# Kernel optimization log

Measured on AMD Instinct MI355X. Metric: run time of the kernel, lower is better.

The kernel has to match this reference:

```python
import jax, jax.numpy as jnp
import numpy as np

B, F, M, C = 4096, 2048, 14, 100
K = 2 ** M  # 16384 latent binary codes


def _codebook(m):
    # itertools.product([0,1], repeat=m) order: row i is binary repr of i, MSB first
    i = jnp.arange(2 ** m)
    j = jnp.arange(m)
    return ((i[:, None] >> (m - 1 - j)[None, :]) & 1).astype(jnp.float32)  # [K, m]


def setup_inputs() -> dict:
    key = jax.random.key(0)
    k1, k2, k3, k4, k5, k6 = jax.random.split(key, 6)
    init_a = 2.0 / np.sqrt(F)
    init_b = 2.0 / np.sqrt(M)
    return {
        "x_in": jax.random.normal(k1, (B, F), dtype=jnp.float32),
        "y_in": jax.random.randint(k2, (B,), 0, C),
        "alpha_0": jax.random.normal(k3, (M,), dtype=jnp.float32),
        "alpha": init_a * jax.random.normal(k4, (M, F), dtype=jnp.float32),
        "beta_0": jax.random.normal(k5, (C,), dtype=jnp.float32),
        "beta": init_b * jax.random.normal(k6, (C, M), dtype=jnp.float32),
    }


def reference(x_in, y_in, alpha_0, alpha, beta_0, beta):
    cb = _codebook(M)  # [K, M]
    # linear_eta
    le = alpha_0[None, :] + x_in @ alpha.T  # [B, M]
    # linear_pi over all codes (mod_codes = 2*cb - 1)
    linear_pi = beta_0[:, None] + beta @ (2.0 * cb - 1.0).T  # [C, K]
    pi = jax.nn.softmax(linear_pi, axis=0)  # exp / sum over classes
    # P(Z|X): exp(cb @ le.T - sum_j softplus(le)) transposed -> [B, K]
    sp = jax.nn.softplus(le)  # log(1 + exp(le)), stable  [B, M]
    P_ZgivenX = jnp.exp((cb @ le.T - jnp.sum(sp, axis=1)[None, :]).T)  # [B, K]
    y1 = jax.nn.one_hot(y_in, C, dtype=le.dtype)  # [B, C]
    numerator = (y1 @ pi) * P_ZgivenX  # [B, K]
    denom = jnp.sum(numerator, axis=1)  # [B]
    # E[Ind Z_j]: masked sum over codes with bit j == 1 == single matmul with cb
    E_IndZ = (numerator @ cb) / denom[:, None]  # [B, M]
    # EI
    EZ = 2.0 * E_IndZ - 1.0
    EI = jnp.sum(y1 * (beta_0[None, :] + EZ @ beta.T))
    # EII
    prob_log = numerator / denom[:, None]
    log_terms = jax.scipy.special.logsumexp(linear_pi, axis=0)  # [K]
    EII = jnp.sum(prob_log * log_terms[None, :])
    # EIII, EIV
    EIII = jnp.sum(E_IndZ * le)
    EIV = jnp.sum(sp)
    return EI - EII + EIII - EIV
```

## Files before the change

kernel.cpp:

```cpp
#include <hip/hip_runtime.h>
#include <math.h>

#define NB 4096
#define NF 2048
#define NM 14
#define NC 100
#define NK 16384

__device__ __forceinline__ float softplus_f(float v) {
    return fmaxf(v, 0.f) + log1pf(__expf(-fabsf(v)));
}

extern "C" __global__ void __launch_bounds__(256) k1_le(
        const float* __restrict__ x, const float* __restrict__ alpha,
        float* __restrict__ le_part) {
    const int tid = threadIdx.x;
    const int wave = tid >> 6, lane = tid & 63;
    const int grp = blockIdx.x >> 1;
    const int half = blockIdx.x & 1;
    const int row0 = grp * 16 + wave * 4;
    const float4* __restrict__ x4 = (const float4*)x;
    const float4* __restrict__ a4 = (const float4*)alpha;
    float acc[4][NM];
#pragma unroll
    for (int r = 0; r < 4; ++r)
#pragma unroll
        for (int j = 0; j < NM; ++j) acc[r][j] = 0.f;
#pragma unroll 1
    for (int cc = 0; cc < 4; ++cc) {
        const int f4i = half * 256 + cc * 64 + lane;
        float4 av[NM];
#pragma unroll
        for (int j = 0; j < NM; ++j) av[j] = a4[j * 512 + f4i];
#pragma unroll
        for (int r = 0; r < 4; ++r) {
            const float4 xv = x4[(row0 + r) * 512 + f4i];
#pragma unroll
            for (int j = 0; j < NM; ++j) {
                acc[r][j] = fmaf(xv.x, av[j].x, acc[r][j]);
                acc[r][j] = fmaf(xv.y, av[j].y, acc[r][j]);
                acc[r][j] = fmaf(xv.z, av[j].z, acc[r][j]);
                acc[r][j] = fmaf(xv.w, av[j].w, acc[r][j]);
            }
        }
    }
#pragma unroll
    for (int m = 1; m < 64; m <<= 1) {
#pragma unroll
        for (int r = 0; r < 4; ++r)
#pragma unroll
            for (int j = 0; j < NM; ++j)
                acc[r][j] += __shfl_xor(acc[r][j], m, 64);
    }
    if (lane == 0) {
        float* dst = le_part + half * (NB * NM) + row0 * NM;
#pragma unroll
        for (int r = 0; r < 4; ++r)
#pragma unroll
            for (int j = 0; j < NM; ++j)
                dst[r * NM + j] = acc[r][j];
    }
}

extern "C" __global__ void __launch_bounds__(256) k2_sl(
        const float* __restrict__ beta, const float* __restrict__ beta0,
        float2* __restrict__ SL) {
    __shared__ float b2[NC * NM];
    __shared__ float base_s[NC];
    __shared__ float Sp[4][64];
    const int tid = threadIdx.x;
    for (int i = tid; i < NC * NM; i += 256) b2[i] = 2.f * beta[i];
    if (tid < NC) {
        float s = beta0[tid];
        for (int j = 0; j < NM; ++j) s -= beta[tid * NM + j];
        base_s[tid] = s;
    }
    __syncthreads();
    const int kl = tid & 63, q = tid >> 6;
    const int k = blockIdx.x * 64 + kl;
    float bits[NM];
#pragma unroll
    for (int j = 0; j < NM; ++j) bits[j] = (float)((k >> (13 - j)) & 1);
    float S = 0.f;
    for (int c = q * 25; c < q * 25 + 25; ++c) {
        float d = base_s[c];
#pragma unroll
        for (int j = 0; j < NM; ++j) d = fmaf(bits[j], b2[c * NM + j], d);
        S += __expf(d);
    }
    Sp[q][kl] = S;
    __syncthreads();
    if (tid < 64) {
        const float Sf = Sp[0][tid] + Sp[1][tid] + Sp[2][tid] + Sp[3][tid];
        SL[blockIdx.x * 64 + tid] = make_float2(1.f / Sf, __logf(Sf));
    }
}

extern "C" __global__ void __launch_bounds__(256) k3_main(
        const float* __restrict__ le_part, const float* __restrict__ alpha0,
        const int* __restrict__ y, const float* __restrict__ beta,
        const float* __restrict__ beta0, const float2* __restrict__ SL,
        float* __restrict__ partial) {
    __shared__ float t_s[8][16];
    __shared__ float sp_s[8][16];
    __shared__ float cs_s[8];
    __shared__ float f_s[8];
    __shared__ float Alds[128][8];
    __shared__ float Elds[128][8];
    __shared__ float red[4][16];
    const int tid = threadIdx.x;
    const int b0 = blockIdx.x * 8;

    if (tid < 128) {
        const int r = tid >> 4, j = tid & 15;
        if (j < NM) {
            const int yv = y[b0 + r];
            const float lv = le_part[(b0 + r) * NM + j]
                           + le_part[NB * NM + (b0 + r) * NM + j] + alpha0[j];
            t_s[r][j] = lv + 2.f * beta[yv * NM + j];
            sp_s[r][j] = softplus_f(lv);
        }
    }
    __syncthreads();
    if (tid < 8) {
        const int yv = y[b0 + tid];
        float cs = beta0[yv];
        for (int j = 0; j < NM; ++j) {
            cs -= beta[yv * NM + j];
            cs += fmaxf(t_s[tid][j], 0.f) - sp_s[tid][j];
        }
        cs_s[tid] = cs;
    }
#pragma unroll
    for (int e = 0; e < 4; ++e) {
        const int idx = tid + 256 * e;
        const int r = idx & 7, h = idx >> 3;
        float A = 0.f, ub = 0.f;
#pragma unroll
        for (int j = 0; j < 7; ++j) {
            const float tv = t_s[r][j];
            A += ((h >> (6 - j)) & 1) ? tv : 0.f;
            ub += fmaxf(tv, 0.f);
        }
        const float Ap = A - ub;
        Alds[h][r] = Ap;
        Elds[h][r] = __expf(Ap);
    }
    const int l = tid & 127;
    float eb[8], aterm[8];
#pragma unroll
    for (int r = 0; r < 8; ++r) {
        float A = 0.f, ub = 0.f;
#pragma unroll
        for (int j = 7; j < NM; ++j) {
            const float tv = t_s[r][j];
            A += ((l >> (13 - j)) & 1) ? tv : 0.f;
            ub += fmaxf(tv, 0.f);
        }
        aterm[r] = A - ub;
        eb[r] = __expf(A - ub);
    }
    __syncthreads();

    float U[8], V[8];
#pragma unroll
    for (int r = 0; r < 8; ++r) { U[r] = 0.f; V[r] = 0.f; }
    const int c = tid >> 7;
#pragma unroll 4
    for (int i = 0; i < 64; ++i) {
        const float2 sl = SL[i * 256 + tid];
        const int h = 2 * i + c;
        const float4 Aa = *(const float4*)&Alds[h][0];
        const float4 Ab = *(const float4*)&Alds[h][4];
        const float4 Ea = *(const float4*)&Elds[h][0];
        const float4 Eb = *(const float4*)&Elds[h][4];
        const float Ar[8] = {Aa.x, Aa.y, Aa.z, Aa.w, Ab.x, Ab.y, Ab.z, Ab.w};
        const float Er[8] = {Ea.x, Ea.y, Ea.z, Ea.w, Eb.x, Eb.y, Eb.z, Eb.w};
#pragma unroll
        for (int r = 0; r < 8; ++r) {
            const float rest = Er[r] * sl.x;
            U[r] += rest;
            V[r] = fmaf(rest, Ar[r] - sl.y, V[r]);
        }
    }
    float vals[16];
#pragma unroll
    for (int r = 0; r < 8; ++r) {
        vals[r] = eb[r] * U[r];
        vals[8 + r] = eb[r] * fmaf(aterm[r], U[r], V[r]);
    }
#pragma unroll
    for (int m = 1; m < 64; m <<= 1)
#pragma unroll
        for (int q2 = 0; q2 < 16; ++q2)
            vals[q2] += __shfl_xor(vals[q2], m, 64);
    const int wv = tid >> 6, lane = tid & 63;
    if (lane == 0) {
#pragma unroll
        for (int q2 = 0; q2 < 16; ++q2) red[wv][q2] = vals[q2];
    }
    __syncthreads();
    if (tid < 16)
        red[0][tid] = red[0][tid] + red[1][tid] + red[2][tid] + red[3][tid];
    __syncthreads();
    if (tid < 8)
        f_s[tid] = cs_s[tid] + red[0][8 + tid] / red[0][tid];
    __syncthreads();
    if (tid == 0) {
        float s = 0.f;
#pragma unroll
        for (int r = 0; r < 8; ++r) s += f_s[r];
        partial[blockIdx.x] = s;
    }
}

extern "C" __global__ void __launch_bounds__(256) k4_reduce(
        const float* __restrict__ partial, float* __restrict__ out) {
    __shared__ float red[4];
    const int tid = threadIdx.x;
    float s = partial[tid] + partial[tid + 256];
#pragma unroll
    for (int m = 1; m < 64; m <<= 1) s += __shfl_xor(s, m, 64);
    const int wv = tid >> 6, lane = tid & 63;
    if (lane == 0) red[wv] = s;
    __syncthreads();
    if (tid == 0) out[0] = red[0] + red[1] + red[2] + red[3];
}

extern "C" void kernel_launch(void* const* d_in, const int* in_sizes, int n_in,
                              void* d_out, int out_size, void* d_ws, size_t ws_size,
                              hipStream_t stream) {
    const float* x      = (const float*)d_in[0];
    const int*   y      = (const int*)d_in[1];
    const float* alpha0 = (const float*)d_in[2];
    const float* alpha  = (const float*)d_in[3];
    const float* beta0  = (const float*)d_in[4];
    const float* beta   = (const float*)d_in[5];

    char* ws = (char*)d_ws;
    float*  le_part = (float*)ws;
    float2* SL      = (float2*)(ws + 2 * NB * NM * 4);
    float*  partial = (float*)(ws + 2 * NB * NM * 4 + NK * 8);
    float*  out     = (float*)d_out;

    k1_le<<<512, 256, 0, stream>>>(x, alpha, le_part);
    k2_sl<<<256, 256, 0, stream>>>(beta, beta0, SL);
    k3_main<<<512, 256, 0, stream>>>(le_part, alpha0, y, beta, beta0, SL, partial);
    k4_reduce<<<1, 256, 0, stream>>>(partial, out);
}
```

Before: 122.8 us.

## Merge le and SL kernels, fold final reduce into main, drop Alds

Merges the linear_eta GEMV and the per-code log-sum-exp kernels into one launch split by block index, and replaces the separate reduce kernel with a last-block atomic-counter reduction inside the main kernel. In the main loop it stops loading the A values from shared memory. It instead accumulates per-bit masked sums of the probabilities and rebuilds the V term algebraically after the loop. This removes two launches and halves the LDS traffic in the hot loop, at the cost of more registers (M[6][8]) and a full unroll that may lower occupancy.

```diff
diff --git a/kernel.cpp b/kernel.cpp
--- a/kernel.cpp
+++ b/kernel.cpp
@@ -11,88 +11,90 @@
     return fmaxf(v, 0.f) + log1pf(__expf(-fabsf(v)));
 }
 
-extern "C" __global__ void __launch_bounds__(256) k1_le(
+extern "C" __global__ void __launch_bounds__(256) k12(
         const float* __restrict__ x, const float* __restrict__ alpha,
-        float* __restrict__ le_part) {
-    const int tid = threadIdx.x;
-    const int wave = tid >> 6, lane = tid & 63;
-    const int grp = blockIdx.x >> 1;
-    const int half = blockIdx.x & 1;
-    const int row0 = grp * 16 + wave * 4;
-    const float4* __restrict__ x4 = (const float4*)x;
-    const float4* __restrict__ a4 = (const float4*)alpha;
-    float acc[4][NM];
-#pragma unroll
-    for (int r = 0; r < 4; ++r)
-#pragma unroll
-        for (int j = 0; j < NM; ++j) acc[r][j] = 0.f;
-#pragma unroll 1
-    for (int cc = 0; cc < 4; ++cc) {
-        const int f4i = half * 256 + cc * 64 + lane;
-        float4 av[NM];
-#pragma unroll
-        for (int j = 0; j < NM; ++j) av[j] = a4[j * 512 + f4i];
-#pragma unroll
-        for (int r = 0; r < 4; ++r) {
-            const float4 xv = x4[(row0 + r) * 512 + f4i];
-#pragma unroll
-            for (int j = 0; j < NM; ++j) {
-                acc[r][j] = fmaf(xv.x, av[j].x, acc[r][j]);
-                acc[r][j] = fmaf(xv.y, av[j].y, acc[r][j]);
-                acc[r][j] = fmaf(xv.z, av[j].z, acc[r][j]);
-                acc[r][j] = fmaf(xv.w, av[j].w, acc[r][j]);
-            }
-        }
-    }
-#pragma unroll
-    for (int m = 1; m < 64; m <<= 1) {
-#pragma unroll
-        for (int r = 0; r < 4; ++r)
-#pragma unroll
-            for (int j = 0; j < NM; ++j)
-                acc[r][j] += __shfl_xor(acc[r][j], m, 64);
-    }
-    if (lane == 0) {
-        float* dst = le_part + half * (NB * NM) + row0 * NM;
-#pragma unroll
-        for (int r = 0; r < 4; ++r)
-#pragma unroll
-            for (int j = 0; j < NM; ++j)
-                dst[r * NM + j] = acc[r][j];
-    }
-}
-
-extern "C" __global__ void __launch_bounds__(256) k2_sl(
         const float* __restrict__ beta, const float* __restrict__ beta0,
-        float2* __restrict__ SL) {
+        float* __restrict__ le_part, float2* __restrict__ SL,
+        int* __restrict__ counter) {
     __shared__ float b2[NC * NM];
     __shared__ float base_s[NC];
     __shared__ float Sp[4][64];
     const int tid = threadIdx.x;
-    for (int i = tid; i < NC * NM; i += 256) b2[i] = 2.f * beta[i];
-    if (tid < NC) {
-        float s = beta0[tid];
-        for (int j = 0; j < NM; ++j) s -= beta[tid * NM + j];
-        base_s[tid] = s;
-    }
-    __syncthreads();
-    const int kl = tid & 63, q = tid >> 6;
-    const int k = blockIdx.x * 64 + kl;
-    float bits[NM];
-#pragma unroll
-    for (int j = 0; j < NM; ++j) bits[j] = (float)((k >> (13 - j)) & 1);
-    float S = 0.f;
-    for (int c = q * 25; c < q * 25 + 25; ++c) {
-        float d = base_s[c];
-#pragma unroll
-        for (int j = 0; j < NM; ++j) d = fmaf(bits[j], b2[c * NM + j], d);
-        S += __expf(d);
-    }
-    Sp[q][kl] = S;
-    __syncthreads();
-    if (tid < 64) {
-        const float Sf = Sp[0][tid] + Sp[1][tid] + Sp[2][tid] + Sp[3][tid];
-        SL[blockIdx.x * 64 + tid] = make_float2(1.f / Sf, __logf(Sf));
+
+    if (blockIdx.x < 512) {
+        const int wave = tid >> 6, lane = tid & 63;
+        const int grp = blockIdx.x >> 1;
+        const int half = blockIdx.x & 1;
+        const int row0 = grp * 16 + wave * 4;
+        const float4* __restrict__ x4 = (const float4*)x;
+        const float4* __restrict__ a4 = (const float4*)alpha;
+        float acc[4][NM];
+#pragma unroll
+        for (int r = 0; r < 4; ++r)
+#pragma unroll
+            for (int j = 0; j < NM; ++j) acc[r][j] = 0.f;
+#pragma unroll 1
+        for (int cc = 0; cc < 4; ++cc) {
+            const int f4i = half * 256 + cc * 64 + lane;
+            float4 av[NM];
+#pragma unroll
+            for (int j = 0; j < NM; ++j) av[j] = a4[j * 512 + f4i];
+#pragma unroll
+            for (int r = 0; r < 4; ++r) {
+                const float4 xv = x4[(row0 + r) * 512 + f4i];
+#pragma unroll
+                for (int j = 0; j < NM; ++j) {
+                    acc[r][j] = fmaf(xv.x, av[j].x, acc[r][j]);
+                    acc[r][j] = fmaf(xv.y, av[j].y, acc[r][j]);
+                    acc[r][j] = fmaf(xv.z, av[j].z, acc[r][j]);
+                    acc[r][j] = fmaf(xv.w, av[j].w, acc[r][j]);
+                }
+            }
+        }
+#pragma unroll
+        for (int m = 1; m < 64; m <<= 1) {
+#pragma unroll
+            for (int r = 0; r < 4; ++r)
+#pragma unroll
+                for (int j = 0; j < NM; ++j)
+                    acc[r][j] += __shfl_xor(acc[r][j], m, 64);
+        }
+        if (lane == 0) {
+            float* dst = le_part + half * (NB * NM) + row0 * NM;
+#pragma unroll
+            for (int r = 0; r < 4; ++r)
+#pragma unroll
+                for (int j = 0; j < NM; ++j)
+                    dst[r * NM + j] = acc[r][j];
+        }
+    } else {
+        const int bid = blockIdx.x - 512;
+        if (bid == 0 && tid == 0) *counter = 0;
+        for (int i = tid; i < NC * NM; i += 256) b2[i] = 2.f * beta[i];
+        if (tid < NC) {
+            float s = beta0[tid];
+            for (int j = 0; j < NM; ++j) s -= beta[tid * NM + j];
+            base_s[tid] = s;
+        }
+        __syncthreads();
+        const int kl = tid & 63, q = tid >> 6;
+        const int k = bid * 64 + kl;
+        float bits[NM];
+#pragma unroll
+        for (int j = 0; j < NM; ++j) bits[j] = (float)((k >> (13 - j)) & 1);
+        float S = 0.f;
+        for (int c = q * 25; c < q * 25 + 25; ++c) {
+            float d = base_s[c];
+#pragma unroll
+            for (int j = 0; j < NM; ++j) d = fmaf(bits[j], b2[c * NM + j], d);
+            S += __expf(d);
+        }
+        Sp[q][kl] = S;
+        __syncthreads();
+        if (tid < 64) {
+            const float Sf = Sp[0][tid] + Sp[1][tid] + Sp[2][tid] + Sp[3][tid];
+            SL[bid * 64 + tid] = make_float2(1.f / Sf, __logf(Sf));
+        }
     }
 }
 
@@ -100,14 +102,16 @@
         const float* __restrict__ le_part, const float* __restrict__ alpha0,
         const int* __restrict__ y, const float* __restrict__ beta,
         const float* __restrict__ beta0, const float2* __restrict__ SL,
-        float* __restrict__ partial) {
+        float* __restrict__ partial, int* __restrict__ counter,
+        float* __restrict__ out) {
     __shared__ float t_s[8][16];
     __shared__ float sp_s[8][16];
     __shared__ float cs_s[8];
     __shared__ float f_s[8];
-    __shared__ float Alds[128][8];
     __shared__ float Elds[128][8];
     __shared__ float red[4][16];
+    __shared__ float red2[4];
+    __shared__ int lastflag;
     const int tid = threadIdx.x;
     const int b0 = blockIdx.x * 8;
 
@@ -142,9 +146,7 @@
             A += ((h >> (6 - j)) & 1) ? tv : 0.f;
             ub += fmaxf(tv, 0.f);
         }
-        const float Ap = A - ub;
-        Alds[h][r] = Ap;
-        Elds[h][r] = __expf(Ap);
+        Elds[h][r] = __expf(A - ub);
     }
     const int l = tid & 127;
     float eb[8], aterm[8];
@@ -162,32 +164,50 @@
     }
     __syncthreads();
 
-    float U[8], V[8];
-#pragma unroll
-    for (int r = 0; r < 8; ++r) { U[r] = 0.f; V[r] = 0.f; }
-    const int c = tid >> 7;
-#pragma unroll 4
+    float U[8], Vlog[8], M[6][8];
+#pragma unroll
+    for (int r = 0; r < 8; ++r) {
+        U[r] = 0.f; Vlog[r] = 0.f;
+#pragma unroll
+        for (int j = 0; j < 6; ++j) M[j][r] = 0.f;
+    }
+    const int c = __builtin_amdgcn_readfirstlane(tid >> 7);
+    const float2* __restrict__ slp = SL + tid;
+#pragma unroll
     for (int i = 0; i < 64; ++i) {
-        const float2 sl = SL[i * 256 + tid];
+        const float2 sl = slp[i * 256];
         const int h = 2 * i + c;
-        const float4 Aa = *(const float4*)&Alds[h][0];
-        const float4 Ab = *(const float4*)&Alds[h][4];
         const float4 Ea = *(const float4*)&Elds[h][0];
         const float4 Eb = *(const float4*)&Elds[h][4];
-        const float Ar[8] = {Aa.x, Aa.y, Aa.z, Aa.w, Ab.x, Ab.y, Ab.z, Ab.w};
         const float Er[8] = {Ea.x, Ea.y, Ea.z, Ea.w, Eb.x, Eb.y, Eb.z, Eb.w};
+        float p[8];
 #pragma unroll
         for (int r = 0; r < 8; ++r) {
-            const float rest = Er[r] * sl.x;
-            U[r] += rest;
-            V[r] = fmaf(rest, Ar[r] - sl.y, V[r]);
+            p[r] = Er[r] * sl.x;
+            U[r] += p[r];
+            Vlog[r] = fmaf(p[r], sl.y, Vlog[r]);
+        }
+#pragma unroll
+        for (int j = 0; j < 6; ++j) {
+            if ((i >> (5 - j)) & 1) {
+#pragma unroll
+                for (int r = 0; r < 8; ++r) M[j][r] += p[r];
+            }
         }
     }
     float vals[16];
 #pragma unroll
     for (int r = 0; r < 8; ++r) {
+        float va = fmaf(aterm[r], U[r], -Vlog[r]);
+        float ub = 0.f;
+#pragma unroll
+        for (int j = 0; j < 7; ++j) ub += fmaxf(t_s[r][j], 0.f);
+        va = fmaf(-ub, U[r], va);
+        if (c) va = fmaf(t_s[r][6], U[r], va);
+#pragma unroll
+        for (int j = 0; j < 6; ++j) va = fmaf(t_s[r][j], M[j][r], va);
         vals[r] = eb[r] * U[r];
-        vals[8 + r] = eb[r] * fmaf(aterm[r], U[r], V[r]);
+        vals[8 + r] = eb[r] * va;
     }
 #pragma unroll
     for (int m = 1; m < 64; m <<= 1)
@@ -211,20 +231,19 @@
 #pragma unroll
         for (int r = 0; r < 8; ++r) s += f_s[r];
         partial[blockIdx.x] = s;
-    }
-}
-
-extern "C" __global__ void __launch_bounds__(256) k4_reduce(
-        const float* __restrict__ partial, float* __restrict__ out) {
-    __shared__ float red[4];
-    const int tid = threadIdx.x;
-    float s = partial[tid] + partial[tid + 256];
-#pragma unroll
-    for (int m = 1; m < 64; m <<= 1) s += __shfl_xor(s, m, 64);
-    const int wv = tid >> 6, lane = tid & 63;
-    if (lane == 0) red[wv] = s;
-    __syncthreads();
-    if (tid == 0) out[0] = red[0] + red[1] + red[2] + red[3];
+        __threadfence();
+        lastflag = (atomicAdd(counter, 1) == 511);
+    }
+    __syncthreads();
+    if (lastflag) {
+        __threadfence();
+        float s = partial[tid] + partial[tid + 256];
+#pragma unroll
+        for (int m = 1; m < 64; m <<= 1) s += __shfl_xor(s, m, 64);
+        if (lane == 0) red2[wv] = s;
+        __syncthreads();
+        if (tid == 0) out[0] = red2[0] + red2[1] + red2[2] + red2[3];
+    }
 }
 
 extern "C" void kernel_launch(void* const* d_in, const int* in_sizes, int n_in,
@@ -241,10 +260,10 @@
     float*  le_part = (float*)ws;
     float2* SL      = (float2*)(ws + 2 * NB * NM * 4);
     float*  partial = (float*)(ws + 2 * NB * NM * 4 + NK * 8);
+    int*    counter = (int*)(ws + 2 * NB * NM * 4 + NK * 8 + 512 * 4);
     float*  out     = (float*)d_out;
 
-    k1_le<<<512, 256, 0, stream>>>(x, alpha, le_part);
-    k2_sl<<<256, 256, 0, stream>>>(beta, beta0, SL);
-    k3_main<<<512, 256, 0, stream>>>(le_part, alpha0, y, beta, beta0, SL, partial);
-    k4_reduce<<<1, 256, 0, stream>>>(partial, out);
-}
+    k12<<<768, 256, 0, stream>>>(x, alpha, beta, beta0, le_part, SL, counter);
+    k3_main<<<512, 256, 0, stream>>>(le_part, alpha0, y, beta, beta0, SL,
+                                     partial, counter, out);
+}
```

Result: no change. 123.4 us (+0.5%).
